# Kernel optimization log

Hardware: AMD Instinct MI355X
Metric: run time of the kernel (lower is better)

The kernel has to match this reference:

```python
import jax, jax.numpy as jnp
import numpy as np


def _gather(feat, idx):
    # feat: [B, L, F], idx: [B, L, D] -> [B, L, D, F]  (per-molecule neighbor gather)
    return jax.vmap(lambda f, i: f[i])(feat, idx)


def setup_inputs() -> dict:
    key = jax.random.key(0)
    ks = jax.random.split(key, 16)
    B, L, D, F, FA, FB, R = 256, 128, 6, 200, 39, 10, 2
    s = 0.05
    return {
        "atom_list": jax.random.normal(ks[0], (B, L, FA), jnp.float32),
        "bond_list": jax.random.normal(ks[1], (B, L, FB), jnp.float32),
        "atom_degree": jax.random.randint(ks[2], (B, L, D), 0, L, jnp.int32),
        "bond_degree": jax.random.randint(ks[3], (B, L, D), 0, L, jnp.int32),
        "atom_W": jax.random.normal(ks[4], (F, FA), jnp.float32) * s,
        "atom_b": jax.random.normal(ks[5], (F,), jnp.float32) * s,
        "nbr_W": jax.random.normal(ks[6], (F, FA + FB), jnp.float32) * s,
        "nbr_b": jax.random.normal(ks[7], (F,), jnp.float32) * s,
        "align_W": jax.random.normal(ks[8], (R, 1, 2 * F), jnp.float32) * s,
        "align_b": jax.random.normal(ks[9], (R, 1), jnp.float32) * s,
        "attend_W": jax.random.normal(ks[10], (R, F, F), jnp.float32) * s,
        "attend_b": jax.random.normal(ks[11], (R, F), jnp.float32) * s,
        "gru_Wih": jax.random.normal(ks[12], (R, 3 * F, F), jnp.float32) * s,
        "gru_Whh": jax.random.normal(ks[13], (R, 3 * F, F), jnp.float32) * s,
        "gru_bih": jax.random.normal(ks[14], (R, 3 * F), jnp.float32) * s,
        "gru_bhh": jax.random.normal(ks[15], (R, 3 * F), jnp.float32) * s,
    }


def reference(atom_list, bond_list, atom_degree, bond_degree,
              atom_W, atom_b, nbr_W, nbr_b,
              align_W, align_b, attend_W, attend_b,
              gru_Wih, gru_Whh, gru_bih, gru_bhh):
    B, L, _ = atom_list.shape
    F = atom_W.shape[0]
    R = align_W.shape[0]
    pad = L - 1  # padding atom index convention from metaGAT

    # masks over padded neighbor slots: [B, L, D, 1]
    is_pad = (atom_degree == pad)[..., None]
    attend_mask = jnp.where(is_pad, 0.0, 1.0).astype(atom_list.dtype)
    softmax_mask = jnp.where(is_pad, -9e8, 0.0).astype(atom_list.dtype)

    # initial atom / neighbor embeddings
    atom_feat = jax.nn.leaky_relu(atom_list @ atom_W.T + atom_b)          # [B,L,F]
    atom_nbr = _gather(atom_list, atom_degree)                             # [B,L,D,FA]
    bond_nbr = _gather(bond_list, bond_degree)                             # [B,L,D,FB]
    nbr_feat = jax.nn.leaky_relu(
        jnp.concatenate([atom_nbr, bond_nbr], axis=-1) @ nbr_W.T + nbr_b)  # [B,L,D,F]

    cur = atom_feat  # GRU hidden / query features (activated after first step)
    for d in range(R):
        if d > 0:
            nbr_feat = _gather(cur, atom_degree)  # [B,L,D,F]
        cur_exp = jnp.broadcast_to(cur[:, :, None, :], nbr_feat.shape)
        feat_align = jnp.concatenate([cur_exp, nbr_feat], axis=-1)        # [B,L,D,2F]
        score = jax.nn.leaky_relu(feat_align @ align_W[d].T + align_b[d]) # [B,L,D,1]
        score = score + softmax_mask
        attn = jax.nn.softmax(score, axis=-2) * attend_mask               # [B,L,D,1]
        nbr_t = nbr_feat @ attend_W[d].T + attend_b[d]                    # [B,L,D,F]
        context = jax.nn.elu(jnp.sum(attn * nbr_t, axis=-2))              # [B,L,F]

        # GRUCell(input=context, hidden=cur)
        gi = context @ gru_Wih[d].T + gru_bih[d]                          # [B,L,3F]
        gh = cur @ gru_Whh[d].T + gru_bhh[d]                              # [B,L,3F]
        ir, iz, inn = jnp.split(gi, 3, axis=-1)
        hr, hz, hn = jnp.split(gh, 3, axis=-1)
        r = jax.nn.sigmoid(ir + hr)
        z = jax.nn.sigmoid(iz + hz)
        n = jnp.tanh(inn + r * hn)
        h = (1.0 - z) * n + z * cur
        cur = jax.nn.relu(h)  # activated_features for next step
    return cur
```

## Files before the change

kernel.cpp:

```cpp
#include <hip/hip_runtime.h>

#define B_     256
#define L_     128
#define D_     6
#define F_     200
#define FA_    39
#define FB_    10
#define PAD_   127
#define LMASK  127
#define NT     256
#define KC8    (F_/8)
#define NTILE  16
#define NQ     (NTILE * D_)
#define NF     (B_ * L_ * F_)
#define MSZ    (F_ * F_)
#define NNODES (B_ * L_)
#define KP     224
#define KPP    232
#define KSTEPS 7
#define NTL    13
#define FRAG_TOTAL (14 * NTL * KSTEPS * 64)
#define PN2    16
#define NPREP  (NNODES / PN2)
#define NBF    ((FRAG_TOTAL + NT - 1) / NT)

typedef __attribute__((ext_vector_type(8))) short sh8;
typedef __attribute__((ext_vector_type(4))) float f32x4;

__device__ __forceinline__ float lrelu(float x) { return x >= 0.0f ? x : 0.01f * x; }
__device__ __forceinline__ float sigm(float x)  { return 1.0f / (1.0f + __expf(-x)); }
__device__ __forceinline__ float fast_tanh(float x) {
    const float e = __expf(2.0f * x);
    return 1.0f - 2.0f / (e + 1.0f);
}
__device__ __forceinline__ unsigned short f2b(float x) {
    unsigned int u = __float_as_uint(x);
    unsigned int r = (u + 0x7FFFu + ((u >> 16) & 1u)) >> 16;
    return (unsigned short)r;
}
__device__ __forceinline__ float b2f(unsigned short u) {
    return __uint_as_float(((unsigned int)u) << 16);
}
#define AFRAG(arr, ks) (*(const sh8*)&arr[lane & 15][(ks) * 32 + ((lane >> 4) << 3)])
__device__ __forceinline__ sh8 bfrag(const unsigned short* __restrict__ WFr,
                                     int mat, int t, int ks, int lane) {
    return *(const sh8*)(WFr + ((((size_t)mat * NTL + t) * KSTEPS + ks) * 64 + lane) * 8);
}

__global__ __launch_bounds__(NT)
void prep_frags_kernel(const float* __restrict__ atom_list, const float* __restrict__ bond_list,
                       const float* __restrict__ atom_W, const float* __restrict__ atom_b,
                       const float* __restrict__ nbr_W,
                       const float* __restrict__ attend_W,
                       const float* __restrict__ gru_Wih,
                       const float* __restrict__ gru_Whh,
                       unsigned short* __restrict__ cur0b,
                       unsigned short* __restrict__ PA, unsigned short* __restrict__ PB,
                       unsigned short* __restrict__ WF)
{
    __shared__ float wsh[F_ * (FA_ + FB_)];
    const int tid = threadIdx.x;

    if (blockIdx.x >= NPREP) {
        const int i = (blockIdx.x - NPREP) * NT + tid;
        if (i >= FRAG_TOTAL) return;
        const int lane = i & 63;
        int rest = i >> 6;
        const int ks = rest % KSTEPS; rest /= KSTEPS;
        const int t  = rest % NTL;
        const int m  = rest / NTL;
        const int n  = t * 16 + (lane & 15);
        const int k0 = ks * 32 + ((lane >> 4) << 3);
        const int r = m / 7, tt = m - r * 7;
        const float* src;
        if (tt == 0)      src = attend_W + (size_t)r * MSZ;
        else if (tt <= 3) src = gru_Wih + ((size_t)r * 3 + (tt - 1)) * MSZ;
        else              src = gru_Whh + ((size_t)r * 3 + (tt - 4)) * MSZ;
        unsigned short o[8];
        #pragma unroll
        for (int j = 0; j < 8; ++j) {
            const int k = k0 + j;
            const float v = (n < F_ && k < F_) ? src[(size_t)n * F_ + k] : 0.0f;
            o[j] = f2b(v);
        }
        uint4 w;
        w.x = (unsigned int)o[0] | ((unsigned int)o[1] << 16);
        w.y = (unsigned int)o[2] | ((unsigned int)o[3] << 16);
        w.z = (unsigned int)o[4] | ((unsigned int)o[5] << 16);
        w.w = (unsigned int)o[6] | ((unsigned int)o[7] << 16);
        ((uint4*)WF)[i] = w;
        return;
    }

    const int node0 = blockIdx.x * PN2;
    const int f     = tid;
    const bool valid = (f < F_);
    const int fc    = valid ? f : 0;

    float wa[FA_];
    float wn[FA_ + FB_];

    for (int i = tid; i < F_ * FA_; i += NT) wsh[i] = atom_W[i];
    __syncthreads();
    #pragma unroll
    for (int k = 0; k < FA_; ++k) wa[k] = wsh[fc * FA_ + k];
    __syncthreads();
    for (int i = tid; i < F_ * (FA_ + FB_); i += NT) wsh[i] = nbr_W[i];
    __syncthreads();
    #pragma unroll
    for (int k = 0; k < FA_ + FB_; ++k) wn[k] = wsh[fc * (FA_ + FB_) + k];
    __syncthreads();

    {
        const float* asrc = atom_list + (size_t)node0 * FA_;
        for (int i = tid; i < PN2 * FA_; i += NT) wsh[i] = asrc[i];
        const float* bsrc = bond_list + (size_t)node0 * FB_;
        for (int i = tid; i < PN2 * FB_; i += NT) wsh[PN2 * FA_ + i] = bsrc[i];
    }
    __syncthreads();

    const float ab = atom_b[fc];

    for (int n = 0; n < PN2; ++n) {
        const float* __restrict__ ar = &wsh[n * FA_];
        const float* __restrict__ br = &wsh[PN2 * FA_ + n * FB_];
        float accA = ab, accPA = 0.0f, accPB = 0.0f;
        #pragma unroll
        for (int k = 0; k < FA_; ++k) {
            const float a = ar[k];
            accA  += a * wa[k];
            accPA += a * wn[k];
        }
        #pragma unroll
        for (int k = 0; k < FB_; ++k) accPB += br[k] * wn[FA_ + k];
        if (valid) {
            const size_t o = (size_t)(node0 + n) * F_ + f;
            cur0b[o] = f2b(lrelu(accA));
            PA[o]    = f2b(accPA);
            PB[o]    = f2b(accPB);
        }
    }
}

__global__ __launch_bounds__(NT, 4)
void round0_kernel(
    const int*   __restrict__ atom_degree,
    const int*   __restrict__ bond_degree,
    const float* __restrict__ align_W,
    const float* __restrict__ align_b,
    const unsigned short* __restrict__ WF,
    const float* __restrict__ attend_b,
    const float* __restrict__ gru_bih,
    const float* __restrict__ gru_bhh,
    const float* __restrict__ nbr_b,
    const unsigned short* __restrict__ PAb,
    const unsigned short* __restrict__ PBb,
    const unsigned short* __restrict__ cur_inb,
    unsigned short* __restrict__ dstb,
    const float* __restrict__ alW2_next,
    float*       __restrict__ s2_next)
{
    const int bid   = blockIdx.x;
    const int mol   = ((bid >> 6) << 3) | (bid & 7);
    const int tile  = (bid >> 3) & 7;
    const int node0 = mol * L_ + tile * NTILE;
    const int bL    = mol * L_;
    const int tid   = threadIdx.x;
    const int lane  = tid & 63;
    const int wave  = tid >> 6;

    __shared__ __align__(16) unsigned short curb  [NTILE][KPP];
    __shared__ __align__(16) unsigned short mixedb[NTILE][KPP];
    __shared__ __align__(16) unsigned short ctxb  [NTILE][KPP];
    __shared__ __align__(16) float nbrb_s[F_];
    __shared__ __align__(16) float alW2_s[F_];
    __shared__ float sc_s [NQ];
    __shared__ float ps_s [NQ];
    __shared__ float asum_s[NTILE];
    __shared__ float s2acc[NTILE];
    __shared__ int   nidx_s[NQ];
    __shared__ int   bidx_s[NQ];

    for (int idx = tid; idx < NTILE * (KP - F_); idx += NT) {
        const int n = idx / (KP - F_), k = F_ + idx % (KP - F_);
        curb[n][k] = 0; mixedb[n][k] = 0; ctxb[n][k] = 0;
    }
    if (tid < NTILE) s2acc[tid] = 0.0f;
    if (tid < F_) { nbrb_s[tid] = nbr_b[tid]; alW2_s[tid] = align_W[F_ + tid]; }
    if (tid < NQ) {
        const int n = tid / D_, j = tid - n * D_;
        nidx_s[tid] = atom_degree[(node0 + n) * D_ + j] & LMASK;
        bidx_s[tid] = bond_degree[(node0 + n) * D_ + j] & LMASK;
    }
    __syncthreads();

    for (int idx = tid; idx < NTILE * KC8; idx += NT) {
        const int n = idx / KC8, kk = idx - n * KC8;
        *(uint4*)&curb[n][kk * 8] =
            *(const uint4*)(cur_inb + (size_t)(node0 + n) * F_ + kk * 8);
    }
    if (tid < 2 * NQ) {
        const int p = tid >> 1, h = tid & 1;
        const unsigned short* pa = PAb + (size_t)(bL + nidx_s[p]) * F_;
        const unsigned short* pb = PBb + (size_t)(bL + bidx_s[p]) * F_;
        float ps = 0.0f;
        for (int kk = h; kk < KC8; kk += 2) {
            const sh8 pa8 = *(const sh8*)(pa + kk * 8);
            const sh8 pb8 = *(const sh8*)(pb + kk * 8);
            const int c0 = kk * 8;
            #pragma unroll
            for (int e = 0; e < 8; ++e)
                ps += lrelu(b2f((unsigned short)pa8[e]) + b2f((unsigned short)pb8[e])
                            + nbrb_s[c0 + e]) * alW2_s[c0 + e];
        }
        ps += __shfl_xor(ps, 1, 2);
        if (h == 0) ps_s[p] = ps;
    }
    __syncthreads();

    {
        const int n = tid >> 4, sub = tid & 15;
        const unsigned short* crow = cur_inb + (size_t)(node0 + n) * F_;
        float s1 = 0.0f;
        for (int f = sub; f < F_; f += 16) s1 += b2f(crow[f]) * align_W[f];
        s1 += __shfl_xor(s1, 1, 16); s1 += __shfl_xor(s1, 2, 16);
        s1 += __shfl_xor(s1, 4, 16); s1 += __shfl_xor(s1, 8, 16);
        float sc = -3.0e38f;
        int nidx = 0;
        if (sub < D_) {
            nidx = nidx_s[n * D_ + sub];
            sc = lrelu(s1 + ps_s[n * D_ + sub] + align_b[0]);
            if (nidx == PAD_) sc += -9.0e8f;
        }
        float mx = sc;
        mx = fmaxf(mx, __shfl_xor(mx, 1, 8));
        mx = fmaxf(mx, __shfl_xor(mx, 2, 8));
        mx = fmaxf(mx, __shfl_xor(mx, 4, 8));
        const float ex = __expf(sc - mx);
        float ssum = ex;
        ssum += __shfl_xor(ssum, 1, 8);
        ssum += __shfl_xor(ssum, 2, 8);
        ssum += __shfl_xor(ssum, 4, 8);
        const float inv = 1.0f / ssum;
        const float aw = (sub < D_ && nidx != PAD_) ? ex * inv : 0.0f;
        if (sub < D_) sc_s[n * D_ + sub] = aw;
        float as = aw;
        as += __shfl_xor(as, 1, 8);
        as += __shfl_xor(as, 2, 8);
        as += __shfl_xor(as, 4, 8);
        if (sub == 0) asum_s[n] = as;
    }
    __syncthreads();

    for (int idx = tid; idx < NTILE * KC8; idx += NT) {
        const int n = idx / KC8, kk = idx - n * KC8;
        const int c0 = kk * 8;
        float m[8];
        #pragma unroll
        for (int e = 0; e < 8; ++e) m[e] = 0.0f;
        #pragma unroll
        for (int j = 0; j < D_; ++j) {
            const float a = sc_s[n * D_ + j];
            const sh8 pa8 = *(const sh8*)(PAb + (size_t)(bL + nidx_s[n*D_+j]) * F_ + c0);
            const sh8 pb8 = *(const sh8*)(PBb + (size_t)(bL + bidx_s[n*D_+j]) * F_ + c0);
            #pragma unroll
            for (int e = 0; e < 8; ++e)
                m[e] += a * lrelu(b2f((unsigned short)pa8[e])
                                + b2f((unsigned short)pb8[e]) + nbrb_s[c0 + e]);
        }
        uint4 w;
        w.x = (unsigned int)f2b(m[0]) | ((unsigned int)f2b(m[1]) << 16);
        w.y = (unsigned int)f2b(m[2]) | ((unsigned int)f2b(m[3]) << 16);
        w.z = (unsigned int)f2b(m[4]) | ((unsigned int)f2b(m[5]) << 16);
        w.w = (unsigned int)f2b(m[6]) | ((unsigned int)f2b(m[7]) << 16);
        *(uint4*)&mixedb[n][c0] = w;
    }
    __syncthreads();

    for (int t = wave; t < NTL; t += 4) {
        f32x4 acc = {0.f, 0.f, 0.f, 0.f};
        #pragma unroll
        for (int ks = 0; ks < KSTEPS; ++ks)
            acc = __builtin_amdgcn_mfma_f32_16x16x32_bf16(
                AFRAG(mixedb, ks), bfrag(WF, 0, t, ks, lane), acc, 0, 0, 0);
        const int f = t * 16 + (lane & 15);
        if (f < F_) {
            const float bb = attend_b[f];
            #pragma unroll
            for (int rg = 0; rg < 4; ++rg) {
                const int node = ((lane >> 4) << 2) + rg;
                float c = acc[rg] + asum_s[node] * bb;
                c = (c > 0.0f) ? c : (__expf(c) - 1.0f);
                ctxb[node][f] = f2b(c);
            }
        }
    }
    __syncthreads();

    float s2part[4] = {0.f, 0.f, 0.f, 0.f};
    for (int t = wave; t < NTL; t += 4) {
        f32x4 ar = {0.f,0.f,0.f,0.f}, az = {0.f,0.f,0.f,0.f};
        f32x4 ani = {0.f,0.f,0.f,0.f}, anh = {0.f,0.f,0.f,0.f};
        #pragma unroll
        for (int ks = 0; ks < KSTEPS; ++ks) {
            const sh8 ac = AFRAG(ctxb, ks);
            const sh8 ah = AFRAG(curb, ks);
            ar  = __builtin_amdgcn_mfma_f32_16x16x32_bf16(ac, bfrag(WF,1,t,ks,lane), ar, 0,0,0);
            ar  = __builtin_amdgcn_mfma_f32_16x16x32_bf16(ah, bfrag(WF,4,t,ks,lane), ar, 0,0,0);
            az  = __builtin_amdgcn_mfma_f32_16x16x32_bf16(ac, bfrag(WF,2,t,ks,lane), az, 0,0,0);
            az  = __builtin_amdgcn_mfma_f32_16x16x32_bf16(ah, bfrag(WF,5,t,ks,lane), az, 0,0,0);
            ani = __builtin_amdgcn_mfma_f32_16x16x32_bf16(ac, bfrag(WF,3,t,ks,lane), ani, 0,0,0);
            anh = __builtin_amdgcn_mfma_f32_16x16x32_bf16(ah, bfrag(WF,6,t,ks,lane), anh, 0,0,0);
        }
        const int f = t * 16 + (lane & 15);
        if (f < F_) {
            const float bir = gru_bih[f],        bhr = gru_bhh[f];
            const float biz = gru_bih[F_ + f],   bhz = gru_bhh[F_ + f];
            const float bin = gru_bih[2*F_ + f], bhn = gru_bhh[2*F_ + f];
            const float w2 = alW2_next[f];
            #pragma unroll
            for (int rg = 0; rg < 4; ++rg) {
                const int node = ((lane >> 4) << 2) + rg;
                const float r  = sigm(ar[rg] + bir + bhr);
                const float z  = sigm(az[rg] + biz + bhz);
                const float nn = fast_tanh(ani[rg] + bin + r * (anh[rg] + bhn));
                const size_t o = (size_t)(node0 + node) * F_ + f;
                const float cv = b2f(cur_inb[o]);
                const float h  = fmaxf((1.0f - z) * nn + z * cv, 0.0f);
                dstb[o] = f2b(h);
                s2part[rg] += h * w2;
            }
        }
    }

    #pragma unroll
    for (int rg = 0; rg < 4; ++rg) {
        float v = s2part[rg];
        v += __shfl_xor(v, 1, 16); v += __shfl_xor(v, 2, 16);
        v += __shfl_xor(v, 4, 16); v += __shfl_xor(v, 8, 16);
        if ((lane & 15) == 0) atomicAdd(&s2acc[((lane >> 4) << 2) + rg], v);
    }
    __syncthreads();
    if (tid < NTILE) s2_next[node0 + tid] = s2acc[tid];
}

__global__ __launch_bounds__(NT, 4)
void round1_kernel(
    const int*   __restrict__ atom_degree,
    const float* __restrict__ align_W,
    const float* __restrict__ align_b,
    const unsigned short* __restrict__ WF,
    const float* __restrict__ attend_b,
    const float* __restrict__ gru_bih,
    const float* __restrict__ gru_bhh,
    const float* __restrict__ s2_tab,
    const unsigned short* __restrict__ cur_inb,
    float*       __restrict__ dst)
{
    const int bid   = blockIdx.x;
    const int mol   = ((bid >> 6) << 3) | (bid & 7);
    const int tile  = (bid >> 3) & 7;
    const int node0 = mol * L_ + tile * NTILE;
    const int bL    = mol * L_;
    const int tid   = threadIdx.x;
    const int lane  = tid & 63;
    const int wave  = tid >> 6;

    __shared__ __align__(16) unsigned short curb  [NTILE][KPP];
    __shared__ __align__(16) unsigned short mixedb[NTILE][KPP];
    __shared__ __align__(16) unsigned short ctxb  [NTILE][KPP];
    __shared__ float sc_s [NQ];
    __shared__ float asum_s[NTILE];
    __shared__ int   nidx_s[NQ];

    for (int idx = tid; idx < NTILE * (KP - F_); idx += NT) {
        const int n = idx / (KP - F_), k = F_ + idx % (KP - F_);
        curb[n][k] = 0; mixedb[n][k] = 0; ctxb[n][k] = 0;
    }

    for (int idx = tid; idx < NTILE * KC8; idx += NT) {
        const int n = idx / KC8, kk = idx - n * KC8;
        *(uint4*)&curb[n][kk * 8] =
            *(const uint4*)(cur_inb + (size_t)(node0 + n) * F_ + kk * 8);
    }

    {
        const int n = tid >> 4, sub = tid & 15;
        const unsigned short* crow = cur_inb + (size_t)(node0 + n) * F_;
        float s1 = 0.0f;
        for (int f = sub; f < F_; f += 16) s1 += b2f(crow[f]) * align_W[f];
        s1 += __shfl_xor(s1, 1, 16); s1 += __shfl_xor(s1, 2, 16);
        s1 += __shfl_xor(s1, 4, 16); s1 += __shfl_xor(s1, 8, 16);
        float sc = -3.0e38f;
        int nidx = 0;
        if (sub < D_) {
            nidx = atom_degree[(node0 + n) * D_ + sub] & LMASK;
            sc = lrelu(s1 + s2_tab[bL + nidx] + align_b[0]);
            if (nidx == PAD_) sc += -9.0e8f;
        }
        float mx = sc;
        mx = fmaxf(mx, __shfl_xor(mx, 1, 8));
        mx = fmaxf(mx, __shfl_xor(mx, 2, 8));
        mx = fmaxf(mx, __shfl_xor(mx, 4, 8));
        const float ex = __expf(sc - mx);
        float ssum = ex;
        ssum += __shfl_xor(ssum, 1, 8);
        ssum += __shfl_xor(ssum, 2, 8);
        ssum += __shfl_xor(ssum, 4, 8);
        const float inv = 1.0f / ssum;
        const float aw = (sub < D_ && nidx != PAD_) ? ex * inv : 0.0f;
        if (sub < D_) {
            sc_s[n * D_ + sub]   = aw;
            nidx_s[n * D_ + sub] = nidx;
        }
        float as = aw;
        as += __shfl_xor(as, 1, 8);
        as += __shfl_xor(as, 2, 8);
        as += __shfl_xor(as, 4, 8);
        if (sub == 0) asum_s[n] = as;
    }
    __syncthreads();

    for (int idx = tid; idx < NTILE * KC8; idx += NT) {
        const int n = idx / KC8, kk = idx - n * KC8;
        const int c0 = kk * 8;
        float m[8];
        #pragma unroll
        for (int e = 0; e < 8; ++e) m[e] = 0.0f;
        #pragma unroll
        for (int j = 0; j < D_; ++j) {
            const float a = sc_s[n * D_ + j];
            const sh8 v8 = *(const sh8*)(cur_inb + (size_t)(bL + nidx_s[n*D_+j]) * F_ + c0);
            #pragma unroll
            for (int e = 0; e < 8; ++e)
                m[e] += a * b2f((unsigned short)v8[e]);
        }
        uint4 w;
        w.x = (unsigned int)f2b(m[0]) | ((unsigned int)f2b(m[1]) << 16);
        w.y = (unsigned int)f2b(m[2]) | ((unsigned int)f2b(m[3]) << 16);
        w.z = (unsigned int)f2b(m[4]) | ((unsigned int)f2b(m[5]) << 16);
        w.w = (unsigned int)f2b(m[6]) | ((unsigned int)f2b(m[7]) << 16);
        *(uint4*)&mixedb[n][c0] = w;
    }
    __syncthreads();

    for (int t = wave; t < NTL; t += 4) {
        f32x4 acc = {0.f, 0.f, 0.f, 0.f};
        #pragma unroll
        for (int ks = 0; ks < KSTEPS; ++ks)
            acc = __builtin_amdgcn_mfma_f32_16x16x32_bf16(
                AFRAG(mixedb, ks), bfrag(WF, 0, t, ks, lane), acc, 0, 0, 0);
        const int f = t * 16 + (lane & 15);
        if (f < F_) {
            const float bb = attend_b[f];
            #pragma unroll
            for (int rg = 0; rg < 4; ++rg) {
                const int node = ((lane >> 4) << 2) + rg;
                float c = acc[rg] + asum_s[node] * bb;
                c = (c > 0.0f) ? c : (__expf(c) - 1.0f);
                ctxb[node][f] = f2b(c);
            }
        }
    }
    __syncthreads();

    for (int t = wave; t < NTL; t += 4) {
        f32x4 ar = {0.f,0.f,0.f,0.f}, az = {0.f,0.f,0.f,0.f};
        f32x4 ani = {0.f,0.f,0.f,0.f}, anh = {0.f,0.f,0.f,0.f};
        #pragma unroll
        for (int ks = 0; ks < KSTEPS; ++ks) {
            const sh8 ac = AFRAG(ctxb, ks);
            const sh8 ah = AFRAG(curb, ks);
            ar  = __builtin_amdgcn_mfma_f32_16x16x32_bf16(ac, bfrag(WF,1,t,ks,lane), ar, 0,0,0);
            ar  = __builtin_amdgcn_mfma_f32_16x16x32_bf16(ah, bfrag(WF,4,t,ks,lane), ar, 0,0,0);
            az  = __builtin_amdgcn_mfma_f32_16x16x32_bf16(ac, bfrag(WF,2,t,ks,lane), az, 0,0,0);
            az  = __builtin_amdgcn_mfma_f32_16x16x32_bf16(ah, bfrag(WF,5,t,ks,lane), az, 0,0,0);
            ani = __builtin_amdgcn_mfma_f32_16x16x32_bf16(ac, bfrag(WF,3,t,ks,lane), ani, 0,0,0);
            anh = __builtin_amdgcn_mfma_f32_16x16x32_bf16(ah, bfrag(WF,6,t,ks,lane), anh, 0,0,0);
        }
        const int f = t * 16 + (lane & 15);
        if (f < F_) {
            const float bir = gru_bih[f],        bhr = gru_bhh[f];
            const float biz = gru_bih[F_ + f],   bhz = gru_bhh[F_ + f];
            const float bin = gru_bih[2*F_ + f], bhn = gru_bhh[2*F_ + f];
            #pragma unroll
            for (int rg = 0; rg < 4; ++rg) {
                const int node = ((lane >> 4) << 2) + rg;
                const float r  = sigm(ar[rg] + bir + bhr);
                const float z  = sigm(az[rg] + biz + bhz);
                const float nn = fast_tanh(ani[rg] + bin + r * (anh[rg] + bhn));
                const size_t o = (size_t)(node0 + node) * F_ + f;
                const float cv = b2f(cur_inb[o]);
                dst[o] = fmaxf((1.0f - z) * nn + z * cv, 0.0f);
            }
        }
    }
}

extern "C" __attribute__((visibility("default")))
void kernel_launch(void* const* d_in, const int* in_sizes, int n_in,
                   void* d_out, int out_size, void* d_ws, size_t ws_size,
                   hipStream_t stream) {
    const float* atom_list = (const float*)d_in[0];
    const float* bond_list = (const float*)d_in[1];
    const int*   atom_deg  = (const int*)d_in[2];
    const int*   bond_deg  = (const int*)d_in[3];
    const float* atom_W    = (const float*)d_in[4];
    const float* atom_b    = (const float*)d_in[5];
    const float* nbr_W     = (const float*)d_in[6];
    const float* nbr_b     = (const float*)d_in[7];
    const float* align_W   = (const float*)d_in[8];
    const float* align_b   = (const float*)d_in[9];
    const float* attend_W  = (const float*)d_in[10];
    const float* attend_b  = (const float*)d_in[11];
    const float* gru_Wih   = (const float*)d_in[12];
    const float* gru_Whh   = (const float*)d_in[13];
    const float* gru_bih   = (const float*)d_in[14];
    const float* gru_bhh   = (const float*)d_in[15];

    float* ws   = (float*)d_ws;
    float* s2b  = ws;
    unsigned short* cur0b = (unsigned short*)(s2b + NNODES);
    unsigned short* cur1b = cur0b + (size_t)NF;
    unsigned short* PAb   = cur1b + (size_t)NF;
    unsigned short* PBb   = PAb   + (size_t)NF;
    unsigned short* WF    = PBb   + (size_t)NF;
    float* out  = (float*)d_out;

    prep_frags_kernel<<<dim3(NPREP + NBF), dim3(NT), 0, stream>>>(
        atom_list, bond_list, atom_W, atom_b, nbr_W,
        attend_W, gru_Wih, gru_Whh,
        cur0b, PAb, PBb, WF);

    const dim3 grid(NNODES / NTILE);
    const size_t rframe = (size_t)7 * NTL * KSTEPS * 64 * 8;

    round0_kernel<<<grid, dim3(NT), 0, stream>>>(
        atom_deg, bond_deg, align_W, align_b,
        WF, attend_b, gru_bih, gru_bhh,
        nbr_b, PAb, PBb, cur0b, cur1b,
        align_W + 2 * F_ + F_, s2b);

    round1_kernel<<<grid, dim3(NT), 0, stream>>>(
        atom_deg, align_W + 2 * F_, align_b + 1,
        WF + rframe, attend_b + F_, gru_bih + 3 * F_, gru_bhh + 3 * F_,
        s2b, cur1b, out);
}
```

Baseline: 328.1 us.

## Precompute round-0 neighbor pair scores in separate kernel; raise MFMA wave priority

Moves the per-pair neighbor align-score dot products out of round0_kernel into a new pair_score_kernel that uses 8 threads per pair across the whole grid. Round0 now reads the precomputed scores from a workspace table, which removes one serial phase where only 192 threads worked, along with a barrier. It also wraps the MFMA loops in s_setprio to favour matrix-issuing waves. The cost is an extra kernel launch and a second read of the PA/PB gathers from global memory.

```diff
diff --git a/kernel.cpp b/kernel.cpp
--- a/kernel.cpp
+++ b/kernel.cpp
@@ -15,6 +15,7 @@
 #define NF     (B_ * L_ * F_)
 #define MSZ    (F_ * F_)
 #define NNODES (B_ * L_)
+#define NPAIRS (NNODES * D_)
 #define KP     224
 #define KPP    232
 #define KSTEPS 7
@@ -142,6 +143,43 @@
     }
 }
 
+#define PPB 32
+__global__ __launch_bounds__(NT)
+void pair_score_kernel(const int* __restrict__ atom_degree,
+                       const int* __restrict__ bond_degree,
+                       const unsigned short* __restrict__ PA,
+                       const unsigned short* __restrict__ PB,
+                       const float* __restrict__ alW2, const float* __restrict__ nbr_b,
+                       float* __restrict__ s2p)
+{
+    __shared__ float w_s[F_], b_s[F_];
+    const int tid = threadIdx.x;
+    if (tid < F_) { w_s[tid] = alW2[tid]; b_s[tid] = nbr_b[tid]; }
+    const int xcd = blockIdx.x & 7;
+    const int j   = blockIdx.x >> 3;
+    const int mol = (j / 24) * 8 + xcd;
+    const int q0  = mol * (L_ * D_) + (j % 24) * PPB;
+    const int q   = q0 + (tid >> 3);
+    const int sub = tid & 7;
+    const int nidx = atom_degree[q] & LMASK;
+    const int bidx = bond_degree[q] & LMASK;
+    const int bL   = mol * L_;
+    const unsigned short* pa = PA + (size_t)(bL + nidx) * F_;
+    const unsigned short* pb = PB + (size_t)(bL + bidx) * F_;
+    __syncthreads();
+    float s = 0.0f;
+    for (int kk = sub; kk < KC8; kk += 8) {
+        const sh8 pa8 = *(const sh8*)(pa + kk * 8);
+        const sh8 pb8 = *(const sh8*)(pb + kk * 8);
+        #pragma unroll
+        for (int e = 0; e < 8; ++e)
+            s += lrelu(b2f((unsigned short)pa8[e]) + b2f((unsigned short)pb8[e])
+                       + b_s[kk * 8 + e]) * w_s[kk * 8 + e];
+    }
+    s += __shfl_xor(s, 1, 8); s += __shfl_xor(s, 2, 8); s += __shfl_xor(s, 4, 8);
+    if (sub == 0) s2p[q] = s;
+}
+
 __global__ __launch_bounds__(NT, 4)
 void round0_kernel(
     const int*   __restrict__ atom_degree,
@@ -155,6 +193,7 @@
     const float* __restrict__ nbr_b,
     const unsigned short* __restrict__ PAb,
     const unsigned short* __restrict__ PBb,
+    const float* __restrict__ s2_tab,
     const unsigned short* __restrict__ cur_inb,
     unsigned short* __restrict__ dstb,
     const float* __restrict__ alW2_next,
@@ -173,9 +212,7 @@
     __shared__ __align__(16) unsigned short mixedb[NTILE][KPP];
     __shared__ __align__(16) unsigned short ctxb  [NTILE][KPP];
     __shared__ __align__(16) float nbrb_s[F_];
-    __shared__ __align__(16) float alW2_s[F_];
     __shared__ float sc_s [NQ];
-    __shared__ float ps_s [NQ];
     __shared__ float asum_s[NTILE];
     __shared__ float s2acc[NTILE];
     __shared__ int   nidx_s[NQ];
@@ -186,37 +223,13 @@
         curb[n][k] = 0; mixedb[n][k] = 0; ctxb[n][k] = 0;
     }
     if (tid < NTILE) s2acc[tid] = 0.0f;
-    if (tid < F_) { nbrb_s[tid] = nbr_b[tid]; alW2_s[tid] = align_W[F_ + tid]; }
-    if (tid < NQ) {
-        const int n = tid / D_, j = tid - n * D_;
-        nidx_s[tid] = atom_degree[(node0 + n) * D_ + j] & LMASK;
-        bidx_s[tid] = bond_degree[(node0 + n) * D_ + j] & LMASK;
-    }
-    __syncthreads();
+    if (tid < F_) nbrb_s[tid] = nbr_b[tid];
 
     for (int idx = tid; idx < NTILE * KC8; idx += NT) {
         const int n = idx / KC8, kk = idx - n * KC8;
         *(uint4*)&curb[n][kk * 8] =
             *(const uint4*)(cur_inb + (size_t)(node0 + n) * F_ + kk * 8);
     }
-    if (tid < 2 * NQ) {
-        const int p = tid >> 1, h = tid & 1;
-        const unsigned short* pa = PAb + (size_t)(bL + nidx_s[p]) * F_;
-        const unsigned short* pb = PBb + (size_t)(bL + bidx_s[p]) * F_;
-        float ps = 0.0f;
-        for (int kk = h; kk < KC8; kk += 2) {
-            const sh8 pa8 = *(const sh8*)(pa + kk * 8);
-            const sh8 pb8 = *(const sh8*)(pb + kk * 8);
-            const int c0 = kk * 8;
-            #pragma unroll
-            for (int e = 0; e < 8; ++e)
-                ps += lrelu(b2f((unsigned short)pa8[e]) + b2f((unsigned short)pb8[e])
-                            + nbrb_s[c0 + e]) * alW2_s[c0 + e];
-        }
-        ps += __shfl_xor(ps, 1, 2);
-        if (h == 0) ps_s[p] = ps;
-    }
-    __syncthreads();
 
     {
         const int n = tid >> 4, sub = tid & 15;
@@ -226,10 +239,11 @@
         s1 += __shfl_xor(s1, 1, 16); s1 += __shfl_xor(s1, 2, 16);
         s1 += __shfl_xor(s1, 4, 16); s1 += __shfl_xor(s1, 8, 16);
         float sc = -3.0e38f;
-        int nidx = 0;
+        int nidx = 0, bidx = 0;
         if (sub < D_) {
-            nidx = nidx_s[n * D_ + sub];
-            sc = lrelu(s1 + ps_s[n * D_ + sub] + align_b[0]);
+            nidx = atom_degree[(node0 + n) * D_ + sub] & LMASK;
+            bidx = bond_degree[(node0 + n) * D_ + sub] & LMASK;
+            sc = lrelu(s1 + s2_tab[(size_t)(node0 + n) * D_ + sub] + align_b[0]);
             if (nidx == PAD_) sc += -9.0e8f;
         }
         float mx = sc;
@@ -243,7 +257,11 @@
         ssum += __shfl_xor(ssum, 4, 8);
         const float inv = 1.0f / ssum;
         const float aw = (sub < D_ && nidx != PAD_) ? ex * inv : 0.0f;
-        if (sub < D_) sc_s[n * D_ + sub] = aw;
+        if (sub < D_) {
+            sc_s[n * D_ + sub]   = aw;
+            nidx_s[n * D_ + sub] = nidx;
+            bidx_s[n * D_ + sub] = bidx;
+        }
         float as = aw;
         as += __shfl_xor(as, 1, 8);
         as += __shfl_xor(as, 2, 8);
@@ -279,10 +297,12 @@
 
     for (int t = wave; t < NTL; t += 4) {
         f32x4 acc = {0.f, 0.f, 0.f, 0.f};
+        __builtin_amdgcn_s_setprio(1);
         #pragma unroll
         for (int ks = 0; ks < KSTEPS; ++ks)
             acc = __builtin_amdgcn_mfma_f32_16x16x32_bf16(
                 AFRAG(mixedb, ks), bfrag(WF, 0, t, ks, lane), acc, 0, 0, 0);
+        __builtin_amdgcn_s_setprio(0);
         const int f = t * 16 + (lane & 15);
         if (f < F_) {
             const float bb = attend_b[f];
@@ -301,6 +321,7 @@
     for (int t = wave; t < NTL; t += 4) {
         f32x4 ar = {0.f,0.f,0.f,0.f}, az = {0.f,0.f,0.f,0.f};
         f32x4 ani = {0.f,0.f,0.f,0.f}, anh = {0.f,0.f,0.f,0.f};
+        __builtin_amdgcn_s_setprio(1);
         #pragma unroll
         for (int ks = 0; ks < KSTEPS; ++ks) {
             const sh8 ac = AFRAG(ctxb, ks);
@@ -312,6 +333,7 @@
             ani = __builtin_amdgcn_mfma_f32_16x16x32_bf16(ac, bfrag(WF,3,t,ks,lane), ani, 0,0,0);
             anh = __builtin_amdgcn_mfma_f32_16x16x32_bf16(ah, bfrag(WF,6,t,ks,lane), anh, 0,0,0);
         }
+        __builtin_amdgcn_s_setprio(0);
         const int f = t * 16 + (lane & 15);
         if (f < F_) {
             const float bir = gru_bih[f],        bhr = gru_bhh[f];
@@ -446,10 +468,12 @@
 
     for (int t = wave; t < NTL; t += 4) {
         f32x4 acc = {0.f, 0.f, 0.f, 0.f};
+        __builtin_amdgcn_s_setprio(1);
         #pragma unroll
         for (int ks = 0; ks < KSTEPS; ++ks)
             acc = __builtin_amdgcn_mfma_f32_16x16x32_bf16(
                 AFRAG(mixedb, ks), bfrag(WF, 0, t, ks, lane), acc, 0, 0, 0);
+        __builtin_amdgcn_s_setprio(0);
         const int f = t * 16 + (lane & 15);
         if (f < F_) {
             const float bb = attend_b[f];
@@ -467,6 +491,7 @@
     for (int t = wave; t < NTL; t += 4) {
         f32x4 ar = {0.f,0.f,0.f,0.f}, az = {0.f,0.f,0.f,0.f};
         f32x4 ani = {0.f,0.f,0.f,0.f}, anh = {0.f,0.f,0.f,0.f};
+        __builtin_amdgcn_s_setprio(1);
         #pragma unroll
         for (int ks = 0; ks < KSTEPS; ++ks) {
             const sh8 ac = AFRAG(ctxb, ks);
@@ -478,6 +503,7 @@
             ani = __builtin_amdgcn_mfma_f32_16x16x32_bf16(ac, bfrag(WF,3,t,ks,lane), ani, 0,0,0);
             anh = __builtin_amdgcn_mfma_f32_16x16x32_bf16(ah, bfrag(WF,6,t,ks,lane), anh, 0,0,0);
         }
+        __builtin_amdgcn_s_setprio(0);
         const int f = t * 16 + (lane & 15);
         if (f < F_) {
             const float bir = gru_bih[f],        bhr = gru_bhh[f];
@@ -520,7 +546,8 @@
 
     float* ws   = (float*)d_ws;
     float* s2b  = ws;
-    unsigned short* cur0b = (unsigned short*)(s2b + NNODES);
+    float* s2p  = s2b + NNODES;
+    unsigned short* cur0b = (unsigned short*)(s2p + NPAIRS);
     unsigned short* cur1b = cur0b + (size_t)NF;
     unsigned short* PAb   = cur1b + (size_t)NF;
     unsigned short* PBb   = PAb   + (size_t)NF;
@@ -532,13 +559,16 @@
         attend_W, gru_Wih, gru_Whh,
         cur0b, PAb, PBb, WF);
 
+    pair_score_kernel<<<dim3(NPAIRS / PPB), dim3(NT), 0, stream>>>(
+        atom_deg, bond_deg, PAb, PBb, align_W + F_, nbr_b, s2p);
+
     const dim3 grid(NNODES / NTILE);
     const size_t rframe = (size_t)7 * NTL * KSTEPS * 64 * 8;
 
     round0_kernel<<<grid, dim3(NT), 0, stream>>>(
         atom_deg, bond_deg, align_W, align_b,
         WF, attend_b, gru_bih, gru_bhh,
-        nbr_b, PAb, PBb, cur0b, cur1b,
+        nbr_b, PAb, PBb, s2p, cur0b, cur1b,
         align_W + 2 * F_ + F_, s2b);
 
     round1_kernel<<<grid, dim3(NT), 0, stream>>>(
```

Result: no change. 322.7 us (-1.6%).
